# Optimization experiments

Measured on AMD Instinct MI355X. Metric: run time of the kernel, lower is better.

The kernel has to match this reference:

```python
import jax, jax.numpy as jnp
import numpy as np

N = 50000       # nodes
E = 1_600_000   # edges (avg degree 32)
IN = 256        # in_dim
HID = 64        # hidden_dim
HEADS = 2
CLS = 10
NEG_SLOPE = 0.2  # PyG GATConv default leaky_relu slope


def gat_layer(x, edge_index, W, att_src, att_dst, bias, heads, concat):
    """PyG-style GATConv (eval mode, add_self_loops=True).
    x: [N, F_in]; W: [F_in, heads*C]; att_src/att_dst: [heads, C]; bias: [heads*C] or [C].
    """
    n = x.shape[0]
    loop = jnp.arange(n)
    src = jnp.concatenate([edge_index[0], loop])   # message sources j
    dst = jnp.concatenate([edge_index[1], loop])   # message targets i
    C = W.shape[1] // heads
    h = (x @ W).reshape(n, heads, C)               # [N, H, C]
    a_s = jnp.sum(h * att_src, axis=-1)            # [N, H]
    a_d = jnp.sum(h * att_dst, axis=-1)            # [N, H]
    e = jax.nn.leaky_relu(a_s[src] + a_d[dst], NEG_SLOPE)   # [E', H]
    # segment softmax over incoming edges of each destination node
    m = jax.lax.stop_gradient(jax.ops.segment_max(e, dst, num_segments=n))
    ex = jnp.exp(e - m[dst])
    denom = jax.ops.segment_sum(ex, dst, num_segments=n)
    alpha = ex / denom[dst]                         # [E', H]
    out = jax.ops.segment_sum(alpha[:, :, None] * h[src], dst, num_segments=n)  # [N, H, C]
    out = out.reshape(n, heads * C) if concat else out.mean(axis=1)
    return out + bias


def setup_inputs() -> dict:
    key = jax.random.key(0)
    ks = jax.random.split(key, 12)
    sd = lambda f: np.float32(1.0 / np.sqrt(f))
    x = jax.random.normal(ks[0], (N, IN), dtype=jnp.float32)
    edge_index = jax.random.randint(ks[1], (2, E), 0, N, dtype=jnp.int64)
    # layer 1: in_dim -> hidden, heads=2, concat
    W1 = jax.random.normal(ks[2], (IN, HEADS * HID), dtype=jnp.float32) * sd(IN)
    as1 = jax.random.normal(ks[3], (HEADS, HID), dtype=jnp.float32) * sd(HID)
    ad1 = jax.random.normal(ks[4], (HEADS, HID), dtype=jnp.float32) * sd(HID)
    b1 = jnp.zeros((HEADS * HID,), dtype=jnp.float32)
    # layer 2: hidden*heads -> hidden, heads=1, concat=False
    W2 = jax.random.normal(ks[5], (HEADS * HID, HID), dtype=jnp.float32) * sd(HEADS * HID)
    as2 = jax.random.normal(ks[6], (1, HID), dtype=jnp.float32) * sd(HID)
    ad2 = jax.random.normal(ks[7], (1, HID), dtype=jnp.float32) * sd(HID)
    b2 = jnp.zeros((HID,), dtype=jnp.float32)
    # linear head
    Wl = jax.random.normal(ks[8], (HID, CLS), dtype=jnp.float32) * sd(HID)
    bl = jnp.zeros((CLS,), dtype=jnp.float32)
    return {"x": x, "edge_index": edge_index,
            "W1": W1, "as1": as1, "ad1": ad1, "b1": b1,
            "W2": W2, "as2": as2, "ad2": ad2, "b2": b2,
            "Wl": Wl, "bl": bl}


def reference(x, edge_index, W1, as1, ad1, b1, W2, as2, ad2, b2, Wl, bl):
    h = jax.nn.elu(gat_layer(x, edge_index, W1, as1, ad1, b1, HEADS, True))
    h = jax.nn.elu(gat_layer(h, edge_index, W2, as2, ad2, b2, 1, False))
    return h @ Wl + bl  # [N, num_classes]
```

## Files before the change

kernel.cpp:

```cpp
#include <hip/hip_runtime.h>

#define NN 50000
#define NE 1600000
#define EP (NE + NN)
#define IN_DIM 256
#define HIDD 64
#define NCLS 10
#define NBKT 196
#define EPB 8192
#define NPB ((EP + EPB - 1) / EPB)
#define BCAP 12288

typedef unsigned short u16;
typedef short bf16x8 __attribute__((ext_vector_type(8)));
typedef float f32x4 __attribute__((ext_vector_type(4)));
typedef unsigned u32x4 __attribute__((ext_vector_type(4)));

__device__ __forceinline__ float b2f(u16 v) { return __uint_as_float(((unsigned)v) << 16); }
__device__ __forceinline__ u16 f2b(float f) {
    unsigned u = __float_as_uint(f);
    unsigned r = (u + 0x7FFFu + ((u >> 16) & 1u)) >> 16;
    return (u16)r;
}

__device__ __forceinline__ void load_edge(const int* __restrict__ ei, int m, int g,
                                          int& s, int& d) {
    if (g < NE) {
        if (m) { s = ei[2 * (size_t)g]; d = ei[2 * ((size_t)NE + g)]; }
        else   { s = ei[g];             d = ei[NE + g]; }
    } else {
        s = d = g - NE;
    }
    s = s < 0 ? 0 : (s >= NN ? NN - 1 : s);
    d = d < 0 ? 0 : (d >= NN ? NN - 1 : d);
}

__device__ __forceinline__ void wcvt_att_job(
    const float* __restrict__ W, const float* __restrict__ as,
    const float* __restrict__ ad, int K, int N, int H, u16* __restrict__ Wt,
    int idx) {
    if (idx >= K * (N + 16)) return;
    int n = idx / K, k = idx - n * K;
    if (n < N) { Wt[idx] = f2b(W[(size_t)k * N + n]); return; }
    int j = n - N;
    if (j >= 2 * H) { Wt[idx] = 0; return; }
    const float* att = (j & 1) ? ad : as;
    int h = j >> 1, C = N / H;
    float sum = 0.f;
    for (int c = 0; c < C; ++c)
        sum += W[(size_t)k * N + h * C + c] * att[h * C + c];
    Wt[idx] = f2b(sum);
}

__global__ __launch_bounds__(1024) void partition_k(
    const int* __restrict__ ei, int* __restrict__ gcursor,
    unsigned* __restrict__ bbuf,
    const float* __restrict__ W1, const float* __restrict__ as1,
    const float* __restrict__ ad1, u16* __restrict__ w1t,
    const float* __restrict__ W2, const float* __restrict__ as2,
    const float* __restrict__ ad2, u16* __restrict__ w2t) {
    __shared__ int hist[NBKT], base[NBKT], cur[NBKT];
    __shared__ unsigned stash[EPB];
    __shared__ int smode;
    int t = threadIdx.x, b = blockIdx.x;
    if (b < 36) wcvt_att_job(W1, as1, ad1, 256, 128, 2, w1t, b * 1024 + t);
    else if (b < 46) wcvt_att_job(W2, as2, ad2, 128, 64, 1, w2t, (b - 36) * 1024 + t);
    if (t < 64) {
        int nz = 0;
#pragma unroll
        for (int k = 0; k < 4; ++k)
            if (ei[2 * (t * 4 + k) + 1] != 0) nz = 1;
        unsigned long long bal = __ballot(nz);
        if (t == 0) smode = (bal == 0ULL) ? 1 : 0;
    }
    for (int i = t; i < NBKT; i += 1024) hist[i] = 0;
    __syncthreads();
    int m = smode;
    int g0 = b * EPB;
    int gend = min(g0 + EPB, EP);
    for (int g = g0 + t; g < gend; g += 1024) {
        int s, d;
        load_edge(ei, m, g, s, d);
        stash[g - g0] = ((unsigned)s << 16) | (unsigned)d;
        atomicAdd(&hist[d >> 8], 1);
    }
    __syncthreads();
    for (int i = t; i < NBKT; i += 1024) {
        base[i] = hist[i] ? atomicAdd(&gcursor[i], hist[i]) : 0;
        cur[i] = 0;
    }
    __syncthreads();
    int cnt = gend - g0;
    for (int l = t; l < cnt; l += 1024) {
        unsigned p = stash[l];
        int d = p & 0xFFFF;
        int bb = d >> 8;
        int r = base[bb] + atomicAdd(&cur[bb], 1);
        if (r < BCAP)
            bbuf[(size_t)bb * BCAP + r] = ((p >> 16) << 8) | (unsigned)(d & 255);
    }
}

__global__ __launch_bounds__(1024) void bucket_csr_k(const unsigned* __restrict__ bbuf,
                                                     const int* __restrict__ gcursor,
                                                     int* __restrict__ row_ptr,
                                                     u16* __restrict__ csr_src) {
    __shared__ int bsc[256];
    __shared__ int hist[256], scn[256], cur[256];
    __shared__ int se0, scnt, stot;
    int b = blockIdx.x, t = threadIdx.x;
    int v = 0;
    if (t < 256) {
        v = (t < NBKT) ? min(gcursor[t], BCAP) : 0;
        bsc[t] = v;
        hist[t] = 0;
    }
    __syncthreads();
    for (int off = 1; off < 256; off <<= 1) {
        int x = (t < 256 && t >= off) ? bsc[t - off] : 0;
        __syncthreads();
        if (t < 256) bsc[t] += x;
        __syncthreads();
    }
    if (t == b) { se0 = bsc[t] - v; scnt = v; }
    if (t == NBKT - 1) stot = bsc[t];
    __syncthreads();
    int e0 = se0, cnt = scnt;
    const unsigned* bb = bbuf + (size_t)b * BCAP;
    for (int e = t; e < cnt; e += 1024)
        atomicAdd(&hist[bb[e] & 255], 1);
    __syncthreads();
    int hv = 0;
    if (t < 256) { hv = hist[t]; scn[t] = hv; }
    __syncthreads();
    for (int off = 1; off < 256; off <<= 1) {
        int x = (t < 256 && t >= off) ? scn[t - off] : 0;
        __syncthreads();
        if (t < 256) scn[t] += x;
        __syncthreads();
    }
    if (t < 256) {
        int ex = scn[t] - hv;
        int n = b * 256 + t;
        if (n < NN) row_ptr[n] = e0 + ex;
        cur[t] = e0 + ex;
    }
    __syncthreads();
    for (int e = t; e < cnt; e += 1024) {
        unsigned p = bb[e];
        int pos = atomicAdd(&cur[p & 255], 1);
        csr_src[pos] = (u16)(p >> 8);
    }
    if (b == 0 && t == 0) row_ptr[NN] = stot;
}

template <int K, int NF, int H, bool F32A>
__global__ __launch_bounds__(256) void gemm_mfma_att_k(
    const float* __restrict__ Af, const u16* __restrict__ Ab,
    const u16* __restrict__ Wt, u16* __restrict__ C,
    float* __restrict__ a_s, float* __restrict__ a_d) {
    constexpr int NTF = NF / 16, NT = NTF + 1, KS = K / 32;
    const int wave = threadIdx.x >> 6, lane = threadIdx.x & 63;
    const int quad = lane >> 4, l15 = lane & 15;
    const int m0 = blockIdx.x * 64 + wave * 16;
    int rowA = m0 + l15;
    if (rowA >= NN) rowA = NN - 1;
    const float* afp = F32A ? (Af + (size_t)rowA * K + quad * 8) : nullptr;
    const u16*   abp = F32A ? nullptr : (Ab + (size_t)rowA * K + quad * 8);
    const u16* bptr = Wt + (size_t)l15 * K + quad * 8;
    f32x4 acc[NT] = {};
#pragma unroll
    for (int ks = 0; ks < KS; ++ks) {
        bf16x8 af;
        if (F32A) {
            float4 v0 = *(const float4*)(afp + ks * 32);
            float4 v1 = *(const float4*)(afp + ks * 32 + 4);
            af[0] = (short)f2b(v0.x); af[1] = (short)f2b(v0.y);
            af[2] = (short)f2b(v0.z); af[3] = (short)f2b(v0.w);
            af[4] = (short)f2b(v1.x); af[5] = (short)f2b(v1.y);
            af[6] = (short)f2b(v1.z); af[7] = (short)f2b(v1.w);
        } else {
            af = *(const bf16x8*)(abp + ks * 32);
        }
        bf16x8 bf[NT];
#pragma unroll
        for (int nt = 0; nt < NT; ++nt)
            bf[nt] = *(const bf16x8*)(bptr + (size_t)nt * 16 * K + ks * 32);
#pragma unroll
        for (int nt = 0; nt < NT; ++nt)
            acc[nt] = __builtin_amdgcn_mfma_f32_16x16x32_bf16(af, bf[nt], acc[nt], 0, 0, 0);
    }
#pragma unroll
    for (int nt = 0; nt < NTF; ++nt) {
#pragma unroll
        for (int reg = 0; reg < 4; ++reg) {
            int row = m0 + quad * 4 + reg;
            if (row < NN) C[(size_t)row * NF + nt * 16 + l15] = f2b(acc[nt][reg]);
        }
    }
    if (l15 < 2 * H) {
        int h = l15 >> 1;
        float* dst = (l15 & 1) ? a_d : a_s;
#pragma unroll
        for (int reg = 0; reg < 4; ++reg) {
            int row = m0 + quad * 4 + reg;
            if (row < NN) dst[row * H + h] = acc[NTF][reg];
        }
    }
}

template <int CH, int H, bool HEAD>
__global__ __launch_bounds__(256) void gat_gather_k(
    const int* __restrict__ row_ptr, const u16* __restrict__ csr_src,
    const float* __restrict__ a_s, const float* __restrict__ a_d,
    const u16* __restrict__ h, const float* __restrict__ bias,
    u16* __restrict__ outg, const float* __restrict__ Wl,
    const float* __restrict__ bl, float* __restrict__ outh) {
    constexpr int LPR = CH / 8;
    constexpr int G = 64 / LPR;
    constexpr int SH = (CH == 128) ? 8 : 7;
    int n = (blockIdx.x * blockDim.x + threadIdx.x) >> 6;
    int lane = threadIdx.x & 63;
    if (n >= NN) return;
    int r0 = row_ptr[n], r1 = row_ptr[n + 1];
    const int q = lane & (LPR - 1);
    const int g = lane >> ((CH == 128) ? 4 : 3);
    const int g4 = g * 4;
    const unsigned qoff = (unsigned)q * 16u;
    const int shl16 = (q < LPR / 2) ? 16 : 0;
    const unsigned char* h8 = (const unsigned char*)h;

    float adn0, adn1 = 0.f;
    if (H == 2) {
        float2 adv = *(const float2*)(a_d + n * 2);
        adn0 = adv.x; adn1 = adv.y;
    } else {
        adn0 = a_d[n];
    }

    float dh0 = 0.f, dh1 = 0.f;
    float acc[8];
#pragma unroll
    for (int v = 0; v < 8; ++v) acc[v] = 0.f;

    for (int base = r0; base < r1; base += 64) {
        int cnt = min(64, r1 - base);
        int idx = base + lane;
        bool act = idx < r1;
        int sl = act ? (int)csr_src[idx] : 0;
        unsigned pex;
        if (H == 2) {
            float2 av = *(const float2*)(a_s + sl * 2);
            float e0 = av.x + adn0;
            e0 = e0 > 0.f ? e0 : 0.2f * e0;
            e0 = fminf(e0, 60.f);
            float ex0 = act ? __expf(e0) : 0.f;
            dh0 += ex0;
            float e1 = av.y + adn1;
            e1 = e1 > 0.f ? e1 : 0.2f * e1;
            e1 = fminf(e1, 60.f);
            float ex1 = act ? __expf(e1) : 0.f;
            dh1 += ex1;
            pex = (unsigned)f2b(ex0) | ((unsigned)f2b(ex1) << 16);
        } else {
            float e0 = a_s[sl] + adn0;
            e0 = e0 > 0.f ? e0 : 0.2f * e0;
            e0 = fminf(e0, 60.f);
            float ex0 = act ? __expf(e0) : 0.f;
            dh0 += ex0;
            pex = (unsigned)sl | ((unsigned)f2b(ex0) << 16);
        }
        for (int j0 = 0; j0 < cnt; j0 += 4 * G) {
            int per[4], slr[4];
#pragma unroll
            for (int i = 0; i < 4; ++i) {
                int a = ((j0 + i * G) << 2) + g4;
                per[i] = __builtin_amdgcn_ds_bpermute(a, (int)pex);
                if (H == 2) slr[i] = __builtin_amdgcn_ds_bpermute(a, sl);
            }
            u32x4 hv[4];
#pragma unroll
            for (int i = 0; i < 4; ++i) {
                unsigned row = (H == 2) ? (unsigned)slr[i]
                                        : ((unsigned)per[i] & 0xFFFFu);
                hv[i] = *(const u32x4*)(h8 + ((row << SH) + qoff));
            }
#pragma unroll
            for (int i = 0; i < 4; ++i) {
                unsigned ex = (H == 2)
                    ? ((((unsigned)per[i]) << shl16) & 0xFFFF0000u)
                    : (((unsigned)per[i]) & 0xFFFF0000u);
                float exf = __uint_as_float(ex);
#pragma unroll
                for (int d = 0; d < 4; ++d) {
                    unsigned w = hv[i][d];
                    acc[2 * d]     += exf * __uint_as_float(w << 16);
                    acc[2 * d + 1] += exf * __uint_as_float(w & 0xFFFF0000u);
                }
            }
        }
    }

#pragma unroll
    for (int off = 32; off; off >>= 1) dh0 += __shfl_xor(dh0, off);
    float dn = dh0;
    if (H == 2) {
#pragma unroll
        for (int off = 32; off; off >>= 1) dh1 += __shfl_xor(dh1, off);
        dn = (q < LPR / 2) ? dh0 : dh1;
    }
#pragma unroll
    for (int v = 0; v < 8; ++v) {
#pragma unroll
        for (int off = LPR; off < 64; off <<= 1)
            acc[v] += __shfl_xor(acc[v], off);
    }

    if (HEAD) {
        float t01 = (lane & 8) ? acc[1] : acc[0];
        float t23 = (lane & 8) ? acc[3] : acc[2];
        float t45 = (lane & 8) ? acc[5] : acc[4];
        float t67 = (lane & 8) ? acc[7] : acc[6];
        float ta = (lane & 16) ? t23 : t01;
        float tb = (lane & 16) ? t67 : t45;
        float ts = (lane & 32) ? tb : ta;
        int srcl = ((lane & 7) << 3) | (lane >> 3);
        float vsw = __uint_as_float(
            __builtin_amdgcn_ds_bpermute(srcl << 2, __float_as_int(ts)));
        float v0 = vsw / dn + bias[lane];
        v0 = v0 > 0.f ? v0 : expm1f(v0);
#pragma unroll
        for (int cls = 0; cls < NCLS; ++cls) {
            float p = v0 * Wl[lane * NCLS + cls];
#pragma unroll
            for (int off = 32; off; off >>= 1) p += __shfl_xor(p, off);
            if (lane == cls) outh[(size_t)n * NCLS + cls] = p + bl[cls];
        }
    } else {
        if (g == 0) {
            float vv[8];
#pragma unroll
            for (int k = 0; k < 8; ++k) {
                float t = acc[k] / dn + bias[q * 8 + k];
                vv[k] = t > 0.f ? t : expm1f(t);
            }
            u32x4 ov;
#pragma unroll
            for (int d = 0; d < 4; ++d)
                ov[d] = (unsigned)f2b(vv[2 * d]) |
                        ((unsigned)f2b(vv[2 * d + 1]) << 16);
            *(u32x4*)(outg + (size_t)n * CH + q * 8) = ov;
        }
    }
}

extern "C" void kernel_launch(void* const* d_in, const int* in_sizes, int n_in,
                              void* d_out, int out_size, void* d_ws, size_t ws_size,
                              hipStream_t stream) {
    const float* x   = (const float*)d_in[0];
    const int*   ei  = (const int*)d_in[1];
    const float* W1  = (const float*)d_in[2];
    const float* as1 = (const float*)d_in[3];
    const float* ad1 = (const float*)d_in[4];
    const float* b1  = (const float*)d_in[5];
    const float* W2  = (const float*)d_in[6];
    const float* as2 = (const float*)d_in[7];
    const float* ad2 = (const float*)d_in[8];
    const float* b2  = (const float*)d_in[9];
    const float* Wl  = (const float*)d_in[10];
    const float* bl  = (const float*)d_in[11];
    float* out = (float*)d_out;

    float* ws = (float*)d_ws;
    size_t o = 0;
    u16* hb  = (u16*)(ws + o); o += (size_t)NN * 64;
    u16* g1  = (u16*)(ws + o); o += (size_t)NN * 64;
    unsigned* bbuf = (unsigned*)g1;
    u16* w1t = (u16*)(ws + o); o += 144 * 256 / 2;
    u16* w2t = (u16*)(ws + o); o += 80 * 128 / 2;
    float* a_s = ws + o;       o += (size_t)NN * 2;
    float* a_d = ws + o;       o += (size_t)NN * 2;
    int* ints = (int*)(ws + o);
    size_t io = 0;
    int* gcursor  = ints + io; io += NBKT;
    int* row_ptr  = ints + io; io += NN + 1;
    u16* csr_src  = (u16*)(ints + io); io += (EP + 1) / 2;

    hipMemsetAsync(gcursor, 0, NBKT * sizeof(int), stream);
    partition_k<<<NPB, 1024, 0, stream>>>(ei, gcursor, bbuf,
                                          W1, as1, ad1, w1t, W2, as2, ad2, w2t);
    bucket_csr_k<<<NBKT, 1024, 0, stream>>>(bbuf, gcursor, row_ptr, csr_src);

    const int gatherBlocks = (NN + 3) / 4;
    const int gemmBlocks = (NN + 63) / 64;

    gemm_mfma_att_k<256, 128, 2, true><<<gemmBlocks, 256, 0, stream>>>(
        x, nullptr, w1t, hb, a_s, a_d);
    gat_gather_k<128, 2, false><<<gatherBlocks, 256, 0, stream>>>(
        row_ptr, csr_src, a_s, a_d, hb, b1, g1, nullptr, nullptr, nullptr);

    gemm_mfma_att_k<128, 64, 1, false><<<gemmBlocks, 256, 0, stream>>>(
        nullptr, g1, w2t, hb, a_s, a_d);
    gat_gather_k<64, 1, true><<<gatherBlocks, 256, 0, stream>>>(
        row_ptr, csr_src, a_s, a_d, hb, b2, nullptr, Wl, bl, out);
}
```

Measured before the change: 315.4 us.

## Recompute source attention logits in gather from fetched features instead of loading a_s

The gather kernel no longer reads the precomputed per-node a_s array or runs a separate per-edge softmax pass with bpermute broadcasting. It computes each edge's source logit on the fly, as a dot product of the already fetched bf16 feature row with att_src, reduced over 8 lanes with shuffles. The exp, the denominator and the accumulation are then done per lane-group. This removes the random a_s gather and the packed-exp shuffles, at the cost of extra FMAs and shuffles per edge, and it uses bf16-rounded features for the logit.

Result: slower. 361.0 us (+14.5%).

```diff
diff --git a/kernel.cpp b/kernel.cpp
--- a/kernel.cpp
+++ b/kernel.cpp
@@ -212,7 +212,7 @@
 template <int CH, int H, bool HEAD>
 __global__ __launch_bounds__(256) void gat_gather_k(
     const int* __restrict__ row_ptr, const u16* __restrict__ csr_src,
-    const float* __restrict__ a_s, const float* __restrict__ a_d,
+    const float* __restrict__ att_s, const float* __restrict__ a_d,
     const u16* __restrict__ h, const float* __restrict__ bias,
     u16* __restrict__ outg, const float* __restrict__ Wl,
     const float* __restrict__ bl, float* __restrict__ outh) {
@@ -225,20 +225,16 @@
     int r0 = row_ptr[n], r1 = row_ptr[n + 1];
     const int q = lane & (LPR - 1);
     const int g = lane >> ((CH == 128) ? 4 : 3);
-    const int g4 = g * 4;
     const unsigned qoff = (unsigned)q * 16u;
-    const int shl16 = (q < LPR / 2) ? 16 : 0;
     const unsigned char* h8 = (const unsigned char*)h;
 
-    float adn0, adn1 = 0.f;
-    if (H == 2) {
-        float2 adv = *(const float2*)(a_d + n * 2);
-        adn0 = adv.x; adn1 = adv.y;
-    } else {
-        adn0 = a_d[n];
-    }
-
-    float dh0 = 0.f, dh1 = 0.f;
+    float4 av0 = *(const float4*)(att_s + q * 8);
+    float4 av1 = *(const float4*)(att_s + q * 8 + 4);
+    float attv[8] = {av0.x, av0.y, av0.z, av0.w, av1.x, av1.y, av1.z, av1.w};
+
+    float adn = (H == 2) ? a_d[n * 2 + (q >> 3)] : a_d[n];
+
+    float dh = 0.f;
     float acc[8];
 #pragma unroll
     for (int v = 0; v < 8; ++v) acc[v] = 0.f;
@@ -247,68 +243,46 @@
         int cnt = min(64, r1 - base);
         int idx = base + lane;
         bool act = idx < r1;
-        int sl = act ? (int)csr_src[idx] : 0;
-        unsigned pex;
-        if (H == 2) {
-            float2 av = *(const float2*)(a_s + sl * 2);
-            float e0 = av.x + adn0;
-            e0 = e0 > 0.f ? e0 : 0.2f * e0;
-            e0 = fminf(e0, 60.f);
-            float ex0 = act ? __expf(e0) : 0.f;
-            dh0 += ex0;
-            float e1 = av.y + adn1;
-            e1 = e1 > 0.f ? e1 : 0.2f * e1;
-            e1 = fminf(e1, 60.f);
-            float ex1 = act ? __expf(e1) : 0.f;
-            dh1 += ex1;
-            pex = (unsigned)f2b(ex0) | ((unsigned)f2b(ex1) << 16);
-        } else {
-            float e0 = a_s[sl] + adn0;
-            e0 = e0 > 0.f ? e0 : 0.2f * e0;
-            e0 = fminf(e0, 60.f);
-            float ex0 = act ? __expf(e0) : 0.f;
-            dh0 += ex0;
-            pex = (unsigned)sl | ((unsigned)f2b(ex0) << 16);
-        }
+        int slv = act ? ((int)csr_src[idx] | 0x10000) : 0;
         for (int j0 = 0; j0 < cnt; j0 += 4 * G) {
-            int per[4], slr[4];
+            int sr[4];
+#pragma unroll
+            for (int i = 0; i < 4; ++i)
+                sr[i] = __builtin_amdgcn_ds_bpermute((j0 + i * G + g) << 2, slv);
+            u32x4 hv[4];
+#pragma unroll
+            for (int i = 0; i < 4; ++i)
+                hv[i] = *(const u32x4*)(
+                    h8 + (((unsigned)(sr[i] & 0xFFFF) << SH) + qoff));
 #pragma unroll
             for (int i = 0; i < 4; ++i) {
-                int a = ((j0 + i * G) << 2) + g4;
-                per[i] = __builtin_amdgcn_ds_bpermute(a, (int)pex);
-                if (H == 2) slr[i] = __builtin_amdgcn_ds_bpermute(a, sl);
+                float f[8];
+#pragma unroll
+                for (int k = 0; k < 4; ++k) {
+                    unsigned w = hv[i][k];
+                    f[2 * k]     = __uint_as_float(w << 16);
+                    f[2 * k + 1] = __uint_as_float(w & 0xFFFF0000u);
+                }
+                float d = f[0] * attv[0];
+#pragma unroll
+                for (int k = 1; k < 8; ++k) d += f[k] * attv[k];
+                d += __shfl_xor(d, 1);
+                d += __shfl_xor(d, 2);
+                d += __shfl_xor(d, 4);
+                float e = d + adn;
+                e = e > 0.f ? e : 0.2f * e;
+                e = fminf(e, 60.f);
+                float ex = __expf(e);
+                ex = (sr[i] & 0x10000) ? ex : 0.f;
+                dh += ex;
+#pragma unroll
+                for (int k = 0; k < 8; ++k) acc[k] += ex * f[k];
             }
-            u32x4 hv[4];
-#pragma unroll
-            for (int i = 0; i < 4; ++i) {
-                unsigned row = (H == 2) ? (unsigned)slr[i]
-                                        : ((unsigned)per[i] & 0xFFFFu);
-                hv[i] = *(const u32x4*)(h8 + ((row << SH) + qoff));
-            }
-#pragma unroll
-            for (int i = 0; i < 4; ++i) {
-                unsigned ex = (H == 2)
-                    ? ((((unsigned)per[i]) << shl16) & 0xFFFF0000u)
-                    : (((unsigned)per[i]) & 0xFFFF0000u);
-                float exf = __uint_as_float(ex);
-#pragma unroll
-                for (int d = 0; d < 4; ++d) {
-                    unsigned w = hv[i][d];
-                    acc[2 * d]     += exf * __uint_as_float(w << 16);
-                    acc[2 * d + 1] += exf * __uint_as_float(w & 0xFFFF0000u);
-                }
-            }
-        }
-    }
-
-#pragma unroll
-    for (int off = 32; off; off >>= 1) dh0 += __shfl_xor(dh0, off);
-    float dn = dh0;
-    if (H == 2) {
-#pragma unroll
-        for (int off = 32; off; off >>= 1) dh1 += __shfl_xor(dh1, off);
-        dn = (q < LPR / 2) ? dh0 : dh1;
-    }
+        }
+    }
+
+#pragma unroll
+    for (int off = LPR; off < 64; off <<= 1) dh += __shfl_xor(dh, off);
 #pragma unroll
     for (int v = 0; v < 8; ++v) {
 #pragma unroll
@@ -327,7 +301,7 @@
         int srcl = ((lane & 7) << 3) | (lane >> 3);
         float vsw = __uint_as_float(
             __builtin_amdgcn_ds_bpermute(srcl << 2, __float_as_int(ts)));
-        float v0 = vsw / dn + bias[lane];
+        float v0 = vsw / dh + bias[lane];
         v0 = v0 > 0.f ? v0 : expm1f(v0);
 #pragma unroll
         for (int cls = 0; cls < NCLS; ++cls) {
@@ -341,7 +315,7 @@
             float vv[8];
 #pragma unroll
             for (int k = 0; k < 8; ++k) {
-                float t = acc[k] / dn + bias[q * 8 + k];
+                float t = acc[k] / dh + bias[q * 8 + k];
                 vv[k] = t > 0.f ? t : expm1f(t);
             }
             u32x4 ov;
@@ -397,10 +371,10 @@
     gemm_mfma_att_k<256, 128, 2, true><<<gemmBlocks, 256, 0, stream>>>(
         x, nullptr, w1t, hb, a_s, a_d);
     gat_gather_k<128, 2, false><<<gatherBlocks, 256, 0, stream>>>(
-        row_ptr, csr_src, a_s, a_d, hb, b1, g1, nullptr, nullptr, nullptr);
+        row_ptr, csr_src, as1, a_d, hb, b1, g1, nullptr, nullptr, nullptr);
 
     gemm_mfma_att_k<128, 64, 1, false><<<gemmBlocks, 256, 0, stream>>>(
         nullptr, g1, w2t, hb, a_s, a_d);
     gat_gather_k<64, 1, true><<<gatherBlocks, 256, 0, stream>>>(
-        row_ptr, csr_src, a_s, a_d, hb, b2, nullptr, Wl, bl, out);
-}
+        row_ptr, csr_src, as2, a_d, hb, b2, nullptr, Wl, bl, out);
+}
```
